# Kernel tuning notes

Measured on AMD Instinct MI355X. Metric: run time of the kernel, lower is better.

The kernel has to match this reference:

```python
import jax, jax.numpy as jnp
import numpy as np

B, S, DIN, DOUT = 4, 2048, 4096, 4096

def setup_inputs() -> dict:
    key = jax.random.key(0)
    k1, k2, k3 = jax.random.split(key, 3)
    x = jax.random.normal(k1, (B, S, DIN), dtype=jnp.float32)
    # symmetric int8 quantized weights, [out_features, in_features]
    int_weight = jax.random.randint(k2, (DOUT, DIN), -128, 128, dtype=jnp.int32).astype(jnp.int8)
    w_scale = jnp.float32(0.01)  # per-tensor scale, zero-point = 0
    fp_bias = jax.random.normal(k3, (DOUT,), dtype=jnp.float32) * 0.01
    return {"x": x, "int_weight": int_weight, "w_scale": w_scale, "fp_bias": fp_bias}

def reference(x, int_weight, w_scale, fp_bias):
    # Dequantize weight: fp32 = int8 * scale (elementwise), then F.linear: x @ w.T + b
    w = int_weight.astype(jnp.float32) * w_scale  # [DOUT, DIN]
    out = jnp.einsum('bsi,oi->bso', x, w) + fp_bias
    return out
```

## Files before the change

### kernel.cpp

```cpp
#include <hip/hip_runtime.h>
#include <hip/hip_bf16.h>

typedef __attribute__((ext_vector_type(8))) short bf16x8;
typedef __attribute__((ext_vector_type(4))) float f32x4;
typedef __attribute__((ext_vector_type(4))) int i32x4;
typedef __attribute__((ext_vector_type(2))) unsigned int u32x2;
typedef __attribute__((ext_vector_type(4))) unsigned int u32x4;

__device__ __forceinline__ unsigned int f2bf(float f) {
    union { float f; unsigned int u; } v; v.f = f;
    unsigned int u = v.u;
    u += 0x7FFFu + ((u >> 16) & 1u);
    return u >> 16;
}

__device__ __forceinline__ void gl_lds16(const void* gptr, void* lptr) {
    __builtin_amdgcn_global_load_lds(
        (const __attribute__((address_space(1))) unsigned int*)gptr,
        (__attribute__((address_space(3))) unsigned int*)lptr, 16, 0, 0);
}

__global__ __launch_bounds__(256) void convert_x_kernel(
    const float* __restrict__ x, unsigned short* __restrict__ xb, long long n8)
{
    long long i = (long long)blockIdx.x * blockDim.x + threadIdx.x;
    const long long stride = (long long)gridDim.x * blockDim.x;
    for (; i < n8; i += stride) {
        const f32x4* p = (const f32x4*)(x + i * 8);
        f32x4 v0 = p[0], v1 = p[1];
        u32x4 q;
        q[0] = f2bf(v0[0]) | (f2bf(v0[1]) << 16);
        q[1] = f2bf(v0[2]) | (f2bf(v0[3]) << 16);
        q[2] = f2bf(v1[0]) | (f2bf(v1[1]) << 16);
        q[3] = f2bf(v1[2]) | (f2bf(v1[3]) << 16);
        *(u32x4*)(xb + i * 8) = q;
    }
}

__global__ __launch_bounds__(256) void convert_w_kernel(
    const int* __restrict__ w, unsigned short* __restrict__ wb, long long n8)
{
    long long i = (long long)blockIdx.x * blockDim.x + threadIdx.x;
    const long long stride = (long long)gridDim.x * blockDim.x;
    for (; i < n8; i += stride) {
        const i32x4* p = (const i32x4*)(w + i * 8);
        i32x4 v0 = p[0], v1 = p[1];
        u32x4 q;
        q[0] = f2bf((float)v0[0]) | (f2bf((float)v0[1]) << 16);
        q[1] = f2bf((float)v0[2]) | (f2bf((float)v0[3]) << 16);
        q[2] = f2bf((float)v1[0]) | (f2bf((float)v1[1]) << 16);
        q[3] = f2bf((float)v1[2]) | (f2bf((float)v1[3]) << 16);
        *(u32x4*)(wb + i * 8) = q;
    }
}

__global__ __launch_bounds__(512, 2) void gemm256_kernel(
    const unsigned short* __restrict__ A, const unsigned short* __restrict__ Bw,
    const float* __restrict__ wscale, const float* __restrict__ bias,
    float* __restrict__ out, int M, int N, int K)
{
    __shared__ unsigned char lds[131072];

    const int tid  = threadIdx.x;
    const int lane = tid & 63;
    const int wid  = tid >> 6;
    const int wr   = wid >> 1;
    const int wc   = wid & 1;

    const int ntn = N >> 8;
    const int nwg = gridDim.x;
    int bid = blockIdx.x;
    if ((nwg & 7) == 0) {
        const int cpx = nwg >> 3;
        bid = (bid & 7) * cpx + (bid >> 3);
    }
    const int bm = bid / ntn;
    const int bn = bid % ntn;
    const int NT = K >> 6;

    const char* Abase = (const char*)(A  + (size_t)bm * 256 * K);
    const char* Bbase = (const char*)(Bw + (size_t)bn * 256 * K);
    const size_t rowb = (size_t)K * 2;

    const int s_colb = (((lane & 7) ^ (lane >> 3)) << 4);
    const int s_rsub = wid * 8 + (lane >> 3);
    const int s_ldso = wid * 1024 + lane * 16;

    auto stageHalf = [&](const char* gRowBase, char* lhalf) {
#pragma unroll
        for (int q = 0; q < 2; ++q)
            gl_lds16(gRowBase + (size_t)(q * 64 + s_rsub) * rowb + s_colb,
                     lhalf + q * 8192 + s_ldso);
    };
    auto Ag = [&](int kt, int h) { return Abase + (size_t)kt * 128 + (size_t)(h * 128) * rowb; };
    auto Bg = [&](int kt, int h) { return Bbase + (size_t)kt * 128 + (size_t)(h * 128) * rowb; };

    const int arow = (wr * 64  + (lane & 15)) * 128;
    const int brow = (wc * 128 + (lane & 15)) * 128;
    const int csw0 = (((lane >> 4) * 16))      ^ ((lane & 7) << 4);
    const int csw1 = (((lane >> 4) * 16) + 64) ^ ((lane & 7) << 4);

    f32x4 acc[4][8];
#pragma unroll
    for (int mi = 0; mi < 4; ++mi)
#pragma unroll
        for (int ni = 0; ni < 8; ++ni)
            acc[mi][ni] = (f32x4){0.f, 0.f, 0.f, 0.f};

    bf16x8 a0[4], a1[4], bA[4], bB[4];

    stageHalf(Ag(0, 0), (char*)lds + 0);
    stageHalf(Ag(0, 1), (char*)lds + 16384);
    stageHalf(Bg(0, 0), (char*)lds + 32768);
    stageHalf(Bg(0, 1), (char*)lds + 49152);
    if (NT > 1) {
        stageHalf(Ag(1, 0), (char*)lds + 65536);
        stageHalf(Ag(1, 1), (char*)lds + 65536 + 16384);
        asm volatile("s_waitcnt vmcnt(4)" ::: "memory");
    } else {
        asm volatile("s_waitcnt vmcnt(0)" ::: "memory");
    }
    __builtin_amdgcn_sched_barrier(0);
    asm volatile("s_barrier" ::: "memory");
    {
        const char* Al = (const char*)lds;
        const char* Bl = Al + 32768;
#pragma unroll
        for (int fm = 0; fm < 4; ++fm) a0[fm] = *(const bf16x8*)(Al + arow + fm * 2048 + csw0);
#pragma unroll
        for (int fn = 0; fn < 4; ++fn) bA[fn] = *(const bf16x8*)(Bl + brow + fn * 2048 + csw0);
    }

#pragma unroll 2
    for (int kt = 0; kt < NT; ++kt) {
        const int c = kt & 1;
        const char* Al = (const char*)lds + (c << 16);
        const char* Bl = Al + 32768;
        char* nb = (char*)lds + ((c ^ 1) << 16);
        char* cb = (char*)lds + (c << 16);

        if (kt + 1 < NT) stageHalf(Bg(kt + 1, 0), nb + 32768);
#pragma unroll
        for (int fm = 0; fm < 4; ++fm) a1[fm] = *(const bf16x8*)(Al + arow + fm * 2048 + csw1);
#pragma unroll
        for (int fn = 0; fn < 4; ++fn) bB[fn] = *(const bf16x8*)(Bl + brow + (fn + 4) * 2048 + csw0);
        __builtin_amdgcn_s_setprio(1);
#pragma unroll
        for (int fm = 0; fm < 4; ++fm)
#pragma unroll
            for (int fn = 0; fn < 4; ++fn)
                acc[fm][fn] = __builtin_amdgcn_mfma_f32_16x16x32_bf16(a0[fm], bA[fn], acc[fm][fn], 0, 0, 0);
        __builtin_amdgcn_s_setprio(0);

        if (kt + 1 < NT) stageHalf(Bg(kt + 1, 1), nb + 49152);
#pragma unroll
        for (int fn = 0; fn < 4; ++fn) bA[fn] = *(const bf16x8*)(Bl + brow + fn * 2048 + csw1);
        __builtin_amdgcn_s_setprio(1);
#pragma unroll
        for (int fm = 0; fm < 4; ++fm)
#pragma unroll
            for (int fn = 0; fn < 4; ++fn)
                acc[fm][fn + 4] = __builtin_amdgcn_mfma_f32_16x16x32_bf16(a0[fm], bB[fn], acc[fm][fn + 4], 0, 0, 0);
        __builtin_amdgcn_s_setprio(0);
        asm volatile("s_waitcnt lgkmcnt(0)" ::: "memory");
        asm volatile("s_barrier" ::: "memory");

        if (kt + 2 < NT) stageHalf(Ag(kt + 2, 0), cb + 0);
#pragma unroll
        for (int fn = 0; fn < 4; ++fn) bB[fn] = *(const bf16x8*)(Bl + brow + (fn + 4) * 2048 + csw1);
        __builtin_amdgcn_s_setprio(1);
#pragma unroll
        for (int fm = 0; fm < 4; ++fm)
#pragma unroll
            for (int fn = 0; fn < 4; ++fn)
                acc[fm][fn] = __builtin_amdgcn_mfma_f32_16x16x32_bf16(a1[fm], bA[fn], acc[fm][fn], 0, 0, 0);
        __builtin_amdgcn_s_setprio(0);

        if (kt + 2 < NT) stageHalf(Ag(kt + 2, 1), cb + 16384);
        if (kt + 1 < NT) {
            if (kt + 2 < NT) { asm volatile("s_waitcnt vmcnt(4)" ::: "memory"); }
            else             { asm volatile("s_waitcnt vmcnt(0)" ::: "memory"); }
            __builtin_amdgcn_sched_barrier(0);
            asm volatile("s_barrier" ::: "memory");
            const char* nAl = (const char*)nb;
            const char* nBl = (const char*)nb + 32768;
#pragma unroll
            for (int fm = 0; fm < 4; ++fm) a0[fm] = *(const bf16x8*)(nAl + arow + fm * 2048 + csw0);
#pragma unroll
            for (int fn = 0; fn < 4; ++fn) bA[fn] = *(const bf16x8*)(nBl + brow + fn * 2048 + csw0);
        }
        __builtin_amdgcn_s_setprio(1);
#pragma unroll
        for (int fm = 0; fm < 4; ++fm)
#pragma unroll
            for (int fn = 0; fn < 4; ++fn)
                acc[fm][fn + 4] = __builtin_amdgcn_mfma_f32_16x16x32_bf16(a1[fm], bB[fn], acc[fm][fn + 4], 0, 0, 0);
        __builtin_amdgcn_s_setprio(0);
        asm volatile("s_barrier" ::: "memory");
    }

    const float scale = *wscale;
    const int orow0 = bm * 256 + wr * 64  + ((lane >> 4) << 2);
    const int ocol0 = bn * 256 + wc * 128 + (lane & 15);
#pragma unroll
    for (int fn = 0; fn < 8; ++fn) {
        const int col = ocol0 + 16 * fn;
        const float bb = bias[col];
#pragma unroll
        for (int fm = 0; fm < 4; ++fm) {
            const int row0 = orow0 + 16 * fm;
#pragma unroll
            for (int i = 0; i < 4; ++i)
                out[(size_t)(row0 + i) * N + col] = acc[fm][fn][i] * scale + bb;
        }
    }
}

__device__ __forceinline__ int swz(int row, int byte_in_row) {
    return row * 128 + (byte_in_row ^ ((row & 7) << 4));
}

__global__ __launch_bounds__(256) void qlinear_fused_kernel(
    const float* __restrict__ X, const int* __restrict__ W,
    const float* __restrict__ wscale, const float* __restrict__ bias,
    float* __restrict__ out, int M, int N, int K)
{
    __shared__ unsigned char smem[32768];

    const int t    = threadIdx.x;
    const int lane = t & 63;
    const int wid  = t >> 6;
    const int wr   = wid >> 1;
    const int wc   = wid & 1;

    const int ntn = N >> 7;
    const int bm  = blockIdx.x / ntn;
    const int bn  = blockIdx.x % ntn;
    const int NT  = K >> 6;

    const float* Ab = X + (size_t)bm * 128 * K;
    const int*   Bb = W + (size_t)bn * 128 * K;

    const int srow = t >> 4, sc4 = t & 15;

    f32x4 av[8];
    i32x4 bv[8];

    auto loadAB = [&](int kt) {
        const float* Ap = Ab + kt * 64 + sc4 * 4;
#pragma unroll
        for (int l = 0; l < 8; ++l)
            av[l] = *(const f32x4*)(Ap + (size_t)(srow + 16 * l) * K);
        const int* Bp = Bb + kt * 64 + sc4 * 4;
#pragma unroll
        for (int l = 0; l < 8; ++l)
            bv[l] = *(const i32x4*)(Bp + (size_t)(srow + 16 * l) * K);
    };

    auto writeAB = [&]() {
#pragma unroll
        for (int l = 0; l < 8; ++l) {
            const int row = srow + 16 * l;
            u32x2 pk;
            pk[0] = f2bf(av[l][0]) | (f2bf(av[l][1]) << 16);
            pk[1] = f2bf(av[l][2]) | (f2bf(av[l][3]) << 16);
            *(u32x2*)(smem + swz(row, sc4 * 8)) = pk;
        }
#pragma unroll
        for (int l = 0; l < 8; ++l) {
            const int row = srow + 16 * l;
            u32x2 pk;
            pk[0] = f2bf((float)bv[l][0]) | (f2bf((float)bv[l][1]) << 16);
            pk[1] = f2bf((float)bv[l][2]) | (f2bf((float)bv[l][3]) << 16);
            *(u32x2*)(smem + 16384 + swz(row, sc4 * 8)) = pk;
        }
    };

    f32x4 acc[4][4];
#pragma unroll
    for (int mi = 0; mi < 4; ++mi)
#pragma unroll
        for (int ni = 0; ni < 4; ++ni)
            acc[mi][ni] = (f32x4){0.f, 0.f, 0.f, 0.f};

    const int kbyte = (lane >> 4) * 16;
    const int afr   = wr * 64 + (lane & 15);
    const int bfr   = wc * 64 + (lane & 15);

    loadAB(0);

    for (int kt = 0; kt < NT; ++kt) {
        writeAB();
        __syncthreads();
        if (kt + 1 < NT) loadAB(kt + 1);
#pragma unroll
        for (int kk = 0; kk < 2; ++kk) {
            bf16x8 a[4], b[4];
#pragma unroll
            for (int mi = 0; mi < 4; ++mi)
                a[mi] = *(const bf16x8*)(smem + swz(afr + 16 * mi, kk * 64 + kbyte));
#pragma unroll
            for (int ni = 0; ni < 4; ++ni)
                b[ni] = *(const bf16x8*)(smem + 16384 + swz(bfr + 16 * ni, kk * 64 + kbyte));
#pragma unroll
            for (int mi = 0; mi < 4; ++mi)
#pragma unroll
                for (int ni = 0; ni < 4; ++ni)
                    acc[mi][ni] = __builtin_amdgcn_mfma_f32_16x16x32_bf16(
                        a[mi], b[ni], acc[mi][ni], 0, 0, 0);
        }
        __syncthreads();
    }

    const float scale = *wscale;
    const int orow0 = bm * 128 + wr * 64 + ((lane >> 4) << 2);
    const int ocol0 = bn * 128 + wc * 64 + (lane & 15);
#pragma unroll
    for (int ni = 0; ni < 4; ++ni) {
        const int col = ocol0 + 16 * ni;
        const float bb = bias[col];
#pragma unroll
        for (int mi = 0; mi < 4; ++mi) {
            const int row0 = orow0 + 16 * mi;
#pragma unroll
            for (int i = 0; i < 4; ++i)
                out[(size_t)(row0 + i) * N + col] = acc[mi][ni][i] * scale + bb;
        }
    }
}

extern "C" void kernel_launch(void* const* d_in, const int* in_sizes, int n_in,
                              void* d_out, int out_size, void* d_ws, size_t ws_size,
                              hipStream_t stream) {
    const float* x      = (const float*)d_in[0];
    const int*   w      = (const int*)d_in[1];
    const float* wscale = (const float*)d_in[2];
    const float* bias   = (const float*)d_in[3];
    float*       out    = (float*)d_out;

    const int DOUT = in_sizes[3];
    const int DIN  = in_sizes[1] / DOUT;
    const int M    = in_sizes[0] / DIN;

    const size_t xb_bytes = (size_t)M * DIN * 2;
    const size_t wb_bytes = (size_t)DOUT * DIN * 2;

    if (ws_size >= xb_bytes + wb_bytes && (M % 256) == 0 && (DOUT % 256) == 0) {
        unsigned short* xb = (unsigned short*)d_ws;
        unsigned short* wb = (unsigned short*)((char*)d_ws + xb_bytes);

        const long long nx8 = (long long)M * DIN / 8;
        const long long nw8 = (long long)DOUT * DIN / 8;
        convert_x_kernel<<<2048, 256, 0, stream>>>(x, xb, nx8);
        convert_w_kernel<<<2048, 256, 0, stream>>>(w, wb, nw8);

        dim3 grid((M / 256) * (DOUT / 256));
        gemm256_kernel<<<grid, 512, 0, stream>>>(xb, wb, wscale, bias, out, M, DOUT, DIN);
    } else {
        dim3 grid((M / 128) * (DOUT / 128));
        qlinear_fused_kernel<<<grid, 256, 0, stream>>>(x, w, wscale, bias, out, M, DOUT, DIN);
    }
}
```

Before: 285.8 us.

## Triple-buffer B tiles in LDS to prefetch two k-steps ahead

Grows LDS from 128KB to 160KB so B tiles have three rotating buffers while A stays double-buffered. B loads for step kt+2 are now issued at the start of iteration kt, so more global loads are in flight (vmcnt raised from 4 to 8), aiming to hide memory latency better. The catch: a 160KB block allocation plus launch_bounds(512,2) may cut occupancy to one workgroup per CU. The loop is also no longer unrolled by two, because buffer offsets now rotate at runtime.

```diff
diff --git a/kernel.cpp b/kernel.cpp
--- a/kernel.cpp
+++ b/kernel.cpp
@@ -59,7 +59,8 @@
     const float* __restrict__ wscale, const float* __restrict__ bias,
     float* __restrict__ out, int M, int N, int K)
 {
-    __shared__ unsigned char lds[131072];
+    __shared__ unsigned char lds[163840];
+    const int B0OFF = 65536;
 
     const int tid  = threadIdx.x;
     const int lane = tid & 63;
@@ -111,12 +112,14 @@
 
     stageHalf(Ag(0, 0), (char*)lds + 0);
     stageHalf(Ag(0, 1), (char*)lds + 16384);
-    stageHalf(Bg(0, 0), (char*)lds + 32768);
-    stageHalf(Bg(0, 1), (char*)lds + 49152);
+    stageHalf(Bg(0, 0), (char*)lds + B0OFF);
+    stageHalf(Bg(0, 1), (char*)lds + B0OFF + 16384);
     if (NT > 1) {
-        stageHalf(Ag(1, 0), (char*)lds + 65536);
-        stageHalf(Ag(1, 1), (char*)lds + 65536 + 16384);
-        asm volatile("s_waitcnt vmcnt(4)" ::: "memory");
+        stageHalf(Ag(1, 0), (char*)lds + 32768);
+        stageHalf(Ag(1, 1), (char*)lds + 32768 + 16384);
+        stageHalf(Bg(1, 0), (char*)lds + B0OFF + 32768);
+        stageHalf(Bg(1, 1), (char*)lds + B0OFF + 32768 + 16384);
+        asm volatile("s_waitcnt vmcnt(8)" ::: "memory");
     } else {
         asm volatile("s_waitcnt vmcnt(0)" ::: "memory");
     }
@@ -124,22 +127,23 @@
     asm volatile("s_barrier" ::: "memory");
     {
         const char* Al = (const char*)lds;
-        const char* Bl = Al + 32768;
+        const char* Bl = (const char*)lds + B0OFF;
 #pragma unroll
         for (int fm = 0; fm < 4; ++fm) a0[fm] = *(const bf16x8*)(Al + arow + fm * 2048 + csw0);
 #pragma unroll
         for (int fn = 0; fn < 4; ++fn) bA[fn] = *(const bf16x8*)(Bl + brow + fn * 2048 + csw0);
     }
 
-#pragma unroll 2
+    int aoff = 0;
+    int bcur = B0OFF, bnxt = B0OFF + 32768, bnn = B0OFF + 65536;
+
     for (int kt = 0; kt < NT; ++kt) {
-        const int c = kt & 1;
-        const char* Al = (const char*)lds + (c << 16);
-        const char* Bl = Al + 32768;
-        char* nb = (char*)lds + ((c ^ 1) << 16);
-        char* cb = (char*)lds + (c << 16);
-
-        if (kt + 1 < NT) stageHalf(Bg(kt + 1, 0), nb + 32768);
+        const char* Al = (const char*)lds + aoff;
+        const char* Bl = (const char*)lds + bcur;
+        char* Bs2 = (char*)lds + bnn;
+        char* As2 = (char*)lds + aoff;
+
+        if (kt + 2 < NT) stageHalf(Bg(kt + 2, 0), Bs2);
 #pragma unroll
         for (int fm = 0; fm < 4; ++fm) a1[fm] = *(const bf16x8*)(Al + arow + fm * 2048 + csw1);
 #pragma unroll
@@ -152,7 +156,7 @@
                 acc[fm][fn] = __builtin_amdgcn_mfma_f32_16x16x32_bf16(a0[fm], bA[fn], acc[fm][fn], 0, 0, 0);
         __builtin_amdgcn_s_setprio(0);
 
-        if (kt + 1 < NT) stageHalf(Bg(kt + 1, 1), nb + 49152);
+        if (kt + 2 < NT) stageHalf(Bg(kt + 2, 1), Bs2 + 16384);
 #pragma unroll
         for (int fn = 0; fn < 4; ++fn) bA[fn] = *(const bf16x8*)(Bl + brow + fn * 2048 + csw1);
         __builtin_amdgcn_s_setprio(1);
@@ -165,7 +169,7 @@
         asm volatile("s_waitcnt lgkmcnt(0)" ::: "memory");
         asm volatile("s_barrier" ::: "memory");
 
-        if (kt + 2 < NT) stageHalf(Ag(kt + 2, 0), cb + 0);
+        if (kt + 2 < NT) stageHalf(Ag(kt + 2, 0), As2);
 #pragma unroll
         for (int fn = 0; fn < 4; ++fn) bB[fn] = *(const bf16x8*)(Bl + brow + (fn + 4) * 2048 + csw1);
         __builtin_amdgcn_s_setprio(1);
@@ -176,14 +180,14 @@
                 acc[fm][fn] = __builtin_amdgcn_mfma_f32_16x16x32_bf16(a1[fm], bA[fn], acc[fm][fn], 0, 0, 0);
         __builtin_amdgcn_s_setprio(0);
 
-        if (kt + 2 < NT) stageHalf(Ag(kt + 2, 1), cb + 16384);
+        if (kt + 2 < NT) stageHalf(Ag(kt + 2, 1), As2 + 16384);
         if (kt + 1 < NT) {
-            if (kt + 2 < NT) { asm volatile("s_waitcnt vmcnt(4)" ::: "memory"); }
+            if (kt + 2 < NT) { asm volatile("s_waitcnt vmcnt(8)" ::: "memory"); }
             else             { asm volatile("s_waitcnt vmcnt(0)" ::: "memory"); }
             __builtin_amdgcn_sched_barrier(0);
             asm volatile("s_barrier" ::: "memory");
-            const char* nAl = (const char*)nb;
-            const char* nBl = (const char*)nb + 32768;
+            const char* nAl = (const char*)lds + (aoff ^ 32768);
+            const char* nBl = (const char*)lds + bnxt;
 #pragma unroll
             for (int fm = 0; fm < 4; ++fm) a0[fm] = *(const bf16x8*)(nAl + arow + fm * 2048 + csw0);
 #pragma unroll
@@ -197,6 +201,9 @@
                 acc[fm][fn + 4] = __builtin_amdgcn_mfma_f32_16x16x32_bf16(a1[fm], bB[fn], acc[fm][fn + 4], 0, 0, 0);
         __builtin_amdgcn_s_setprio(0);
         asm volatile("s_barrier" ::: "memory");
+
+        aoff ^= 32768;
+        const int tmp = bcur; bcur = bnxt; bnxt = bnn; bnn = tmp;
     }
 
     const float scale = *wscale;
@@ -345,7 +352,8 @@
     const size_t xb_bytes = (size_t)M * DIN * 2;
     const size_t wb_bytes = (size_t)DOUT * DIN * 2;
 
-    if (ws_size >= xb_bytes + wb_bytes && (M % 256) == 0 && (DOUT % 256) == 0) {
+    if (ws_size >= xb_bytes + wb_bytes && (M % 256) == 0 && (DOUT % 256) == 0
+        && (DIN % 64) == 0 && (DIN / 64) >= 2) {
         unsigned short* xb = (unsigned short*)d_ws;
         unsigned short* wb = (unsigned short*)((char*)d_ws + xb_bytes);
 
```

Result: no change. 284.9 us (-0.3%).
